# Kernel tuning notes

Measured on AMD Instinct MI355X. Metric: run time of the kernel, lower is better.

The kernel has to match this reference:

```python
import jax, jax.numpy as jnp
import numpy as np

N, E, D, H, C, L = 50000, 600000, 128, 128, 40, 2
NEG_SLOPE = 0.1


def setup_inputs() -> dict:
    key = jax.random.key(0)
    ks = jax.random.split(key, 12)

    def lin(k, din, dout):
        return (jax.random.normal(k, (din, dout), jnp.float32) / np.sqrt(din)).astype(jnp.float32)

    x = jax.random.normal(ks[0], (N, D), jnp.float32)
    edge_index = jax.random.randint(ks[1], (2, E), 0, N, dtype=jnp.int32)
    return {
        "x": x,
        "edge_index": edge_index,
        "enc_Wl": lin(ks[2], D, H),
        "enc_Wr": lin(ks[3], D, H),
        "enc_b": jnp.zeros((H,), jnp.float32),
        "lay_Wl": jnp.stack([lin(jax.random.fold_in(ks[4], i), H, H) for i in range(L)]),
        "lay_Wr": jnp.stack([lin(jax.random.fold_in(ks[5], i), H, H) for i in range(L)]),
        "lay_b": jnp.zeros((L, H), jnp.float32),
        "dec_Wl": lin(ks[6], H, C),
        "dec_Wr": lin(ks[7], H, C),
        "dec_b": jnp.zeros((C,), jnp.float32),
    }


def _sage(x, src, dst, inv_cnt, Wl, Wr, b):
    # mean-aggregate neighbor messages: gather x[src], scatter-sum to dst, divide by degree
    agg = jax.ops.segment_sum(x[src], dst, num_segments=N) * inv_cnt  # [N, d_in]
    return agg @ Wl + x @ Wr + b


def reference(x, edge_index, enc_Wl, enc_Wr, enc_b, lay_Wl, lay_Wr, lay_b, dec_Wl, dec_Wr, dec_b):
    src, dst = edge_index[0], edge_index[1]
    # in-degree per target node, clamped to 1 (PyG scatter-mean semantics: isolated nodes get 0)
    deg = jax.ops.segment_sum(jnp.ones((E,), jnp.float32), dst, num_segments=N)
    inv_cnt = (1.0 / jnp.maximum(deg, 1.0))[:, None]  # [N, 1]

    h = jax.nn.leaky_relu(_sage(x, src, dst, inv_cnt, enc_Wl, enc_Wr, enc_b), NEG_SLOPE)
    for i in range(L):
        h = jax.nn.leaky_relu(_sage(h, src, dst, inv_cnt, lay_Wl[i], lay_Wr[i], lay_b[i]), NEG_SLOPE)
    out = _sage(h, src, dst, inv_cnt, dec_Wl, dec_Wr, dec_b)
    return jax.nn.log_softmax(out, axis=1)
```

## Files before the change

### kernel.cpp

```cpp
#include <hip/hip_runtime.h>
#include <hip/hip_bf16.h>

#define NN 50000
#define EE 600000
#define HH 128
#define CC 40
#define NEG 0.1f
#define CAP 40

typedef __attribute__((ext_vector_type(8))) short bf16x8;
typedef __attribute__((ext_vector_type(4))) float f32x4;

__device__ __forceinline__ unsigned short f2bf(float f) {
    unsigned u = __float_as_uint(f);
    unsigned r = u + 0x7fffu + ((u >> 16) & 1u);
    return (unsigned short)(r >> 16);
}
__device__ __forceinline__ float bfhi(unsigned v) { return __uint_as_float(v & 0xFFFF0000u); }
__device__ __forceinline__ float bflo(unsigned v) { return __uint_as_float(v << 16); }

__global__ void k_build(const int* __restrict__ src, const int* __restrict__ dst,
                        int* __restrict__ counts, int* __restrict__ csr) {
    int e = blockIdx.x * blockDim.x + threadIdx.x;
    if (e < EE) {
        int d = dst[e];
        if ((unsigned)d < (unsigned)NN) {
            int sl = atomicAdd(&counts[d], 1);
            if (sl < CAP) csr[d * CAP + sl] = src[e];
        }
    }
}

struct PrepArgs {
    const float* wsrc[8];
    unsigned short* wdst[8];
    int* counts;
    const float* x;
    unsigned* xb;
};

template <int DOUT, int DOUTP>
__device__ __forceinline__ void swz_one(const float* __restrict__ W,
                                        unsigned short* __restrict__ dstf, int idx) {
    int k = idx / DOUTP, n = idx % DOUTP;
    unsigned short val = (n < DOUT) ? f2bf(W[k * DOUT + n]) : (unsigned short)0;
    int kt = k >> 5, kin = k & 31, nt = n >> 4, nin = n & 15;
    int lane = ((kin >> 3) << 4) | nin;
    int j = kin & 7;
    int NT = DOUTP >> 4;
    dstf[(((kt * NT + nt) * 64) + lane) * 8 + j] = val;
}

__global__ void k_prep(PrepArgs a) {
    int b = blockIdx.x;
    if (b < 384) {
        int tid = b * 256 + threadIdx.x;
        if (tid < NN) a.counts[tid] = 0;
        int which = b >> 6;
        int idx = (b & 63) * 256 + threadIdx.x;
        swz_one<HH, HH>(a.wsrc[which], a.wdst[which], idx);
    } else if (b < 432) {
        int bb = b - 384;
        int which = 6 + bb / 24;
        int idx = (bb % 24) * 256 + threadIdx.x;
        swz_one<CC, 48>(a.wsrc[which], a.wdst[which], idx);
    } else {
        int t = (b - 432) * 256 + threadIdx.x;
        if (t < NN * HH / 4) {
            float4 v = ((const float4*)a.x)[t];
            uint2 o;
            o.x = ((unsigned)f2bf(v.y) << 16) | f2bf(v.x);
            o.y = ((unsigned)f2bf(v.w) << 16) | f2bf(v.z);
            ((uint2*)a.xb)[t] = o;
        }
    }
}

template <int MODE>
__global__ __launch_bounds__(512) void k_layer(
    const unsigned short* __restrict__ hin,
    const int* __restrict__ counts, const int* __restrict__ csr,
    const unsigned short* __restrict__ B1f, const unsigned short* __restrict__ B2f,
    const float* __restrict__ bias, unsigned short* __restrict__ out,
    const unsigned short* __restrict__ Tf, unsigned short* __restrict__ tOut) {
    __shared__ unsigned lds[16][72];
    int wid = threadIdx.x >> 6;
    int lane = threadIdx.x & 63;
    int m0 = blockIdx.x * 16;
    int g = lane & 7;
    int s = lane >> 3;
    const uint4* hw4 = (const uint4*)hin;

    int beg[2], cnt[2];
    float sc[2];
    int maxd = 0;
#pragma unroll
    for (int n = 0; n < 2; ++n) {
        int node = m0 + wid * 2 + n;
        int c = counts[node];
        c = c < CAP ? c : CAP;
        beg[n] = node * CAP;
        cnt[n] = c;
        sc[n] = 1.0f / (float)(c > 0 ? c : 1);
        maxd = maxd > c ? maxd : c;
    }
    int rounds = (maxd + 7) >> 3;

    for (int ph = 0; ph < 2; ++ph) {
        float acc[2][8];
#pragma unroll
        for (int n = 0; n < 2; ++n)
#pragma unroll
            for (int d = 0; d < 8; ++d) acc[n][d] = 0.f;

        uint4 v[2]; int ok[2];
        auto issue = [&](int r, uint4* vv, int* okk) {
#pragma unroll
            for (int n = 0; n < 2; ++n) {
                int idx = r * 8 + s;
                int o = idx < cnt[n];
                int row = csr[beg[n] + (o ? idx : 0)];
                vv[n] = hw4[(size_t)row * 16 + ph * 8 + g];
                okk[n] = o;
            }
        };
        if (rounds > 0) {
            issue(0, v, ok);
            for (int r = 0; r < rounds; ++r) {
                uint4 vn[2]; int okn[2];
                bool more = (r + 1 < rounds);
                if (more) issue(r + 1, vn, okn);
#pragma unroll
                for (int n = 0; n < 2; ++n) {
                    if (ok[n]) {
                        acc[n][0] += bflo(v[n].x); acc[n][1] += bfhi(v[n].x);
                        acc[n][2] += bflo(v[n].y); acc[n][3] += bfhi(v[n].y);
                        acc[n][4] += bflo(v[n].z); acc[n][5] += bfhi(v[n].z);
                        acc[n][6] += bflo(v[n].w); acc[n][7] += bfhi(v[n].w);
                    }
                }
                if (more) {
#pragma unroll
                    for (int n = 0; n < 2; ++n) { v[n] = vn[n]; ok[n] = okn[n]; }
                }
            }
        }
#pragma unroll
        for (int n = 0; n < 2; ++n) {
#pragma unroll
            for (int d = 0; d < 8; ++d) {
                float t = acc[n][d];
                t += __shfl_xor(t, 8, 64);
                t += __shfl_xor(t, 16, 64);
                t += __shfl_xor(t, 32, 64);
                acc[n][d] = t;
            }
            if (s == 0) {
                uint4 w4;
                w4.x = ((unsigned)f2bf(acc[n][1] * sc[n]) << 16) | f2bf(acc[n][0] * sc[n]);
                w4.y = ((unsigned)f2bf(acc[n][3] * sc[n]) << 16) | f2bf(acc[n][2] * sc[n]);
                w4.z = ((unsigned)f2bf(acc[n][5] * sc[n]) << 16) | f2bf(acc[n][4] * sc[n]);
                w4.w = ((unsigned)f2bf(acc[n][7] * sc[n]) << 16) | f2bf(acc[n][6] * sc[n]);
                *(uint4*)&lds[wid * 2 + n][ph * 32 + g * 4] = w4;
            }
        }
    }
    __syncthreads();

    int nin = lane & 15;
    int kq = lane >> 4;
    const unsigned* arow = &lds[nin][0];

    f32x4 acc1 = (f32x4){0.f, 0.f, 0.f, 0.f};

#pragma unroll
    for (int kt = 0; kt < 4; ++kt) {
        bf16x8 a1 = *(const bf16x8*)(arow + kt * 16 + kq * 4);
        bf16x8 a2 = *(const bf16x8*)(hin + (size_t)(m0 + nin) * HH + kt * 32 + kq * 8);
        bf16x8 b1 = *(const bf16x8*)(B1f + (((kt * 8 + wid) * 64) + lane) * 8);
        acc1 = __builtin_amdgcn_mfma_f32_16x16x32_bf16(a1, b1, acc1, 0, 0, 0);
        bf16x8 b2 = *(const bf16x8*)(B2f + (((kt * 8 + wid) * 64) + lane) * 8);
        acc1 = __builtin_amdgcn_mfma_f32_16x16x32_bf16(a2, b2, acc1, 0, 0, 0);
    }

    int col = wid * 16 + nin;
    float bv = bias[col];
    unsigned short hv[4];
#pragma unroll
    for (int r = 0; r < 4; ++r) {
        int m = m0 + kq * 4 + r;
        float v = acc1[r] + bv;
        v = fmaxf(v, NEG * v);
        hv[r] = f2bf(v);
        out[(size_t)m * HH + col] = hv[r];
    }

    if (MODE == 1) {
        __syncthreads();
        unsigned short* lsh = (unsigned short*)&lds[0][0];
#pragma unroll
        for (int r = 0; r < 4; ++r) lsh[(kq * 4 + r) * 144 + col] = hv[r];
        __syncthreads();
        if (wid < 3) {
            f32x4 at = (f32x4){0.f, 0.f, 0.f, 0.f};
#pragma unroll
            for (int kt = 0; kt < 4; ++kt) {
                bf16x8 a = *(const bf16x8*)&lsh[nin * 144 + kt * 32 + kq * 8];
                bf16x8 b = *(const bf16x8*)(Tf + (((kt * 3 + wid) * 64) + lane) * 8);
                at = __builtin_amdgcn_mfma_f32_16x16x32_bf16(a, b, at, 0, 0, 0);
            }
#pragma unroll
            for (int r = 0; r < 4; ++r) {
                int m = m0 + kq * 4 + r;
                tOut[(size_t)m * 48 + wid * 16 + nin] = f2bf(at[r]);
            }
        }
    }
}

__global__ __launch_bounds__(512) void k_dec(
    const unsigned short* __restrict__ tbuf,
    const unsigned short* __restrict__ h1,
    const int* __restrict__ counts, const int* __restrict__ csr,
    const unsigned short* __restrict__ B2f, const float* __restrict__ bias,
    float* __restrict__ out) {
    __shared__ float aggT[16][52];
    int wid = threadIdx.x >> 6;
    int lane = threadIdx.x & 63;
    int m0 = blockIdx.x * 16;
    int g = lane & 7;
    int g6 = g < 6 ? g : g - 6;
    int s = lane >> 3;
    const uint4* t4 = (const uint4*)tbuf;

    int beg[2], cnt[2];
    float sc[2];
    int maxd = 0;
#pragma unroll
    for (int n = 0; n < 2; ++n) {
        int node = m0 + wid * 2 + n;
        int c = counts[node];
        c = c < CAP ? c : CAP;
        beg[n] = node * CAP;
        cnt[n] = c;
        sc[n] = 1.0f / (float)(c > 0 ? c : 1);
        maxd = maxd > c ? maxd : c;
    }
    int rounds = (maxd + 7) >> 3;

    float acc[2][8];
#pragma unroll
    for (int n = 0; n < 2; ++n)
#pragma unroll
        for (int d = 0; d < 8; ++d) acc[n][d] = 0.f;

    uint4 v[2]; int ok[2];
    auto issue = [&](int r, uint4* vv, int* okk) {
#pragma unroll
        for (int n = 0; n < 2; ++n) {
            int idx = r * 8 + s;
            int o = idx < cnt[n];
            int row = csr[beg[n] + (o ? idx : 0)];
            vv[n] = t4[(size_t)row * 6 + g6];
            okk[n] = o;
        }
    };
    if (rounds > 0) {
        issue(0, v, ok);
        for (int r = 0; r < rounds; ++r) {
            uint4 vn[2]; int okn[2];
            bool more = (r + 1 < rounds);
            if (more) issue(r + 1, vn, okn);
#pragma unroll
            for (int n = 0; n < 2; ++n) {
                if (ok[n]) {
                    acc[n][0] += bflo(v[n].x); acc[n][1] += bfhi(v[n].x);
                    acc[n][2] += bflo(v[n].y); acc[n][3] += bfhi(v[n].y);
                    acc[n][4] += bflo(v[n].z); acc[n][5] += bfhi(v[n].z);
                    acc[n][6] += bflo(v[n].w); acc[n][7] += bfhi(v[n].w);
                }
            }
            if (more) {
#pragma unroll
                for (int n = 0; n < 2; ++n) { v[n] = vn[n]; ok[n] = okn[n]; }
            }
        }
    }
#pragma unroll
    for (int n = 0; n < 2; ++n) {
#pragma unroll
        for (int d = 0; d < 8; ++d) {
            float t = acc[n][d];
            t += __shfl_xor(t, 8, 64);
            t += __shfl_xor(t, 16, 64);
            t += __shfl_xor(t, 32, 64);
            acc[n][d] = t;
        }
        if (s == 0 && g < 6) {
            float4 p0, p1;
            p0.x = acc[n][0] * sc[n]; p0.y = acc[n][1] * sc[n];
            p0.z = acc[n][2] * sc[n]; p0.w = acc[n][3] * sc[n];
            p1.x = acc[n][4] * sc[n]; p1.y = acc[n][5] * sc[n];
            p1.z = acc[n][6] * sc[n]; p1.w = acc[n][7] * sc[n];
            *(float4*)&aggT[wid * 2 + n][8 * g] = p0;
            *(float4*)&aggT[wid * 2 + n][8 * g + 4] = p1;
        }
    }
    __syncthreads();
    if (wid != 0) return;

    int nin = lane & 15, kq = lane >> 4;
    f32x4 acc2[3];
#pragma unroll
    for (int j = 0; j < 3; ++j) acc2[j] = (f32x4){0.f, 0.f, 0.f, 0.f};
#pragma unroll
    for (int kt = 0; kt < 4; ++kt) {
        bf16x8 a2 = *(const bf16x8*)(h1 + (size_t)(m0 + nin) * HH + kt * 32 + kq * 8);
#pragma unroll
        for (int j = 0; j < 3; ++j) {
            bf16x8 b2 = *(const bf16x8*)(B2f + (((kt * 3 + j) * 64) + lane) * 8);
            acc2[j] = __builtin_amdgcn_mfma_f32_16x16x32_bf16(a2, b2, acc2[j], 0, 0, 0);
        }
    }
    float bv[3];
#pragma unroll
    for (int t = 0; t < 3; ++t) {
        int col = t * 16 + nin;
        bv[t] = (col < CC) ? bias[col] : 0.f;
    }
#pragma unroll
    for (int r = 0; r < 4; ++r) {
        int m = m0 + kq * 4 + r;
        int ml = kq * 4 + r;
        float v[3];
        float mx = -1e30f;
#pragma unroll
        for (int t = 0; t < 3; ++t) {
            int col = t * 16 + nin;
            v[t] = acc2[t][r] + aggT[ml][col] + bv[t];
            if (col < CC) mx = fmaxf(mx, v[t]);
        }
        for (int off = 1; off < 16; off <<= 1) mx = fmaxf(mx, __shfl_xor(mx, off, 64));
        float sm = 0.f;
#pragma unroll
        for (int t = 0; t < 3; ++t) {
            int col = t * 16 + nin;
            if (col < CC) sm += expf(v[t] - mx);
        }
        for (int off = 1; off < 16; off <<= 1) sm += __shfl_xor(sm, off, 64);
        float lse = mx + logf(sm);
#pragma unroll
        for (int t = 0; t < 3; ++t) {
            int col = t * 16 + nin;
            if (col < CC) out[(size_t)m * CC + col] = v[t] - lse;
        }
    }
}

extern "C" void kernel_launch(void* const* d_in, const int* in_sizes, int n_in,
                              void* d_out, int out_size, void* d_ws, size_t ws_size,
                              hipStream_t stream) {
    const float* x      = (const float*)d_in[0];
    const int*   ei     = (const int*)d_in[1];
    const float* enc_Wl = (const float*)d_in[2];
    const float* enc_Wr = (const float*)d_in[3];
    const float* enc_b  = (const float*)d_in[4];
    const float* lay_Wl = (const float*)d_in[5];
    const float* lay_Wr = (const float*)d_in[6];
    const float* lay_b  = (const float*)d_in[7];
    const float* dec_Wl = (const float*)d_in[8];
    const float* dec_Wr = (const float*)d_in[9];
    const float* dec_b  = (const float*)d_in[10];
    float* out = (float*)d_out;

    const int* src = ei;
    const int* dst = ei + EE;

    char* p = (char*)d_ws;
    auto carve = [&](size_t bytes) {
        char* r = p;
        p += (bytes + 255) & ~(size_t)255;
        return r;
    };
    int*            counts = (int*)carve(NN * 4);
    int*            csr    = (int*)carve((size_t)NN * CAP * 4);
    unsigned short* h1     = (unsigned short*)carve((size_t)NN * HH * 2);
    unsigned short* h2     = (unsigned short*)carve((size_t)NN * HH * 2);
    unsigned short* tbuf   = (unsigned short*)carve((size_t)NN * 48 * 2 + 256);
    unsigned short* wf[8];
    for (int i = 0; i < 6; ++i) wf[i] = (unsigned short*)carve(HH * HH * 2);
    wf[6] = (unsigned short*)carve(HH * 48 * 2);
    wf[7] = (unsigned short*)carve(HH * 48 * 2);

    {
        PrepArgs a;
        a.wsrc[0] = enc_Wl; a.wsrc[1] = enc_Wr;
        a.wsrc[2] = lay_Wl; a.wsrc[3] = lay_Wr;
        a.wsrc[4] = lay_Wl + HH * HH; a.wsrc[5] = lay_Wr + HH * HH;
        a.wsrc[6] = dec_Wl; a.wsrc[7] = dec_Wr;
        for (int i = 0; i < 8; ++i) a.wdst[i] = wf[i];
        a.counts = counts;
        a.x = x;
        a.xb = (unsigned*)h2;
        k_prep<<<432 + (NN * HH / 4 + 255) / 256, 256, 0, stream>>>(a);
    }

    k_build<<<(EE + 255) / 256, 256, 0, stream>>>(src, dst, counts, csr);

    const int FB = NN / 16;
    k_layer<0><<<FB, 512, 0, stream>>>(h2, counts, csr, wf[0], wf[1], enc_b,      h1, nullptr, nullptr);
    k_layer<0><<<FB, 512, 0, stream>>>(h1, counts, csr, wf[2], wf[3], lay_b,      h2, nullptr, nullptr);
    k_layer<1><<<FB, 512, 0, stream>>>(h2, counts, csr, wf[4], wf[5], lay_b + HH, h1, wf[6], tbuf);

    k_dec<<<FB, 512, 0, stream>>>(tbuf, h1, counts, csr, wf[7], dec_b, out);
}
```

Baseline: 294.2 us.

## Assign one wavefront per node with fully unrolled prefetched neighbor gather

Blocks grow from 512 to 1024 threads, so each of the 16 wavefronts aggregates a single destination node instead of two. In k_layer each lane now reads a whole 256-byte row (16 lanes cover a row, 4 neighbors per round) in one pass rather than two half-row phases. All CSR indices are preloaded into registers and the gather is fully unrolled with three rotating buffers, replacing the dynamic loop bounded by the max degree of a node pair. This aims to raise memory-level parallelism and remove the phase loop and divergence between node pairs. The cost is that half the waves sit idle during the MFMA stage, plus higher register pressure under launch_bounds(1024, 8).

```diff
diff --git a/kernel.cpp b/kernel.cpp
--- a/kernel.cpp
+++ b/kernel.cpp
@@ -77,7 +77,7 @@
 }
 
 template <int MODE>
-__global__ __launch_bounds__(512) void k_layer(
+__global__ __launch_bounds__(1024, 8) void k_layer(
     const unsigned short* __restrict__ hin,
     const int* __restrict__ counts, const int* __restrict__ csr,
     const unsigned short* __restrict__ B1f, const unsigned short* __restrict__ B2f,
@@ -87,119 +87,111 @@
     int wid = threadIdx.x >> 6;
     int lane = threadIdx.x & 63;
     int m0 = blockIdx.x * 16;
-    int g = lane & 7;
-    int s = lane >> 3;
+    int gg = lane & 15;
+    int s = lane >> 4;
     const uint4* hw4 = (const uint4*)hin;
 
-    int beg[2], cnt[2];
-    float sc[2];
-    int maxd = 0;
-#pragma unroll
-    for (int n = 0; n < 2; ++n) {
-        int node = m0 + wid * 2 + n;
-        int c = counts[node];
-        c = c < CAP ? c : CAP;
-        beg[n] = node * CAP;
-        cnt[n] = c;
-        sc[n] = 1.0f / (float)(c > 0 ? c : 1);
-        maxd = maxd > c ? maxd : c;
-    }
-    int rounds = (maxd + 7) >> 3;
-
-    for (int ph = 0; ph < 2; ++ph) {
-        float acc[2][8];
-#pragma unroll
-        for (int n = 0; n < 2; ++n)
-#pragma unroll
-            for (int d = 0; d < 8; ++d) acc[n][d] = 0.f;
-
-        uint4 v[2]; int ok[2];
-        auto issue = [&](int r, uint4* vv, int* okk) {
-#pragma unroll
-            for (int n = 0; n < 2; ++n) {
-                int idx = r * 8 + s;
-                int o = idx < cnt[n];
-                int row = csr[beg[n] + (o ? idx : 0)];
-                vv[n] = hw4[(size_t)row * 16 + ph * 8 + g];
-                okk[n] = o;
-            }
-        };
-        if (rounds > 0) {
-            issue(0, v, ok);
-            for (int r = 0; r < rounds; ++r) {
-                uint4 vn[2]; int okn[2];
-                bool more = (r + 1 < rounds);
-                if (more) issue(r + 1, vn, okn);
-#pragma unroll
-                for (int n = 0; n < 2; ++n) {
-                    if (ok[n]) {
-                        acc[n][0] += bflo(v[n].x); acc[n][1] += bfhi(v[n].x);
-                        acc[n][2] += bflo(v[n].y); acc[n][3] += bfhi(v[n].y);
-                        acc[n][4] += bflo(v[n].z); acc[n][5] += bfhi(v[n].z);
-                        acc[n][6] += bflo(v[n].w); acc[n][7] += bfhi(v[n].w);
-                    }
-                }
-                if (more) {
-#pragma unroll
-                    for (int n = 0; n < 2; ++n) { v[n] = vn[n]; ok[n] = okn[n]; }
-                }
-            }
-        }
-#pragma unroll
-        for (int n = 0; n < 2; ++n) {
-#pragma unroll
-            for (int d = 0; d < 8; ++d) {
-                float t = acc[n][d];
-                t += __shfl_xor(t, 8, 64);
-                t += __shfl_xor(t, 16, 64);
-                t += __shfl_xor(t, 32, 64);
-                acc[n][d] = t;
-            }
-            if (s == 0) {
-                uint4 w4;
-                w4.x = ((unsigned)f2bf(acc[n][1] * sc[n]) << 16) | f2bf(acc[n][0] * sc[n]);
-                w4.y = ((unsigned)f2bf(acc[n][3] * sc[n]) << 16) | f2bf(acc[n][2] * sc[n]);
-                w4.z = ((unsigned)f2bf(acc[n][5] * sc[n]) << 16) | f2bf(acc[n][4] * sc[n]);
-                w4.w = ((unsigned)f2bf(acc[n][7] * sc[n]) << 16) | f2bf(acc[n][6] * sc[n]);
-                *(uint4*)&lds[wid * 2 + n][ph * 32 + g * 4] = w4;
-            }
-        }
+    int node = m0 + wid;
+    int cnt = counts[node];
+    cnt = cnt < CAP ? cnt : CAP;
+    int beg = node * CAP;
+    float sc = 1.0f / (float)(cnt > 0 ? cnt : 1);
+    int sr = (__builtin_amdgcn_readfirstlane(cnt) + 3) >> 2;
+
+    int row[10];
+#pragma unroll
+    for (int r = 0; r < 10; ++r) {
+        int v = csr[beg + r * 4 + s];
+        row[r] = ((unsigned)v < (unsigned)NN) ? v : 0;
+    }
+
+    float acc[8];
+#pragma unroll
+    for (int d = 0; d < 8; ++d) acc[d] = 0.f;
+
+    uint4 vA, vB, vC;
+
+#define ISS(R, V) \
+    if (sr > (R)) V = hw4[((unsigned)row[R] << 4) + gg]
+#define ACC8(R, V)                                            \
+    if (sr > (R)) {                                           \
+        if ((R) * 4 + s < cnt) {                              \
+            acc[0] += bflo(V.x); acc[1] += bfhi(V.x);         \
+            acc[2] += bflo(V.y); acc[3] += bfhi(V.y);         \
+            acc[4] += bflo(V.z); acc[5] += bfhi(V.z);         \
+            acc[6] += bflo(V.w); acc[7] += bfhi(V.w);         \
+        }                                                     \
+    }
+
+    ISS(0, vA); ISS(1, vB); ISS(2, vC);
+    ACC8(0, vA); ISS(3, vA);
+    ACC8(1, vB); ISS(4, vB);
+    ACC8(2, vC); ISS(5, vC);
+    ACC8(3, vA); ISS(6, vA);
+    ACC8(4, vB); ISS(7, vB);
+    ACC8(5, vC); ISS(8, vC);
+    ACC8(6, vA); ISS(9, vA);
+    ACC8(7, vB);
+    ACC8(8, vC);
+    ACC8(9, vA);
+#undef ISS
+#undef ACC8
+
+#pragma unroll
+    for (int d = 0; d < 8; ++d) {
+        float t = acc[d];
+        t += __shfl_xor(t, 16, 64);
+        t += __shfl_xor(t, 32, 64);
+        acc[d] = t * sc;
+    }
+    if (lane < 16) {
+        uint4 w4;
+        w4.x = ((unsigned)f2bf(acc[1]) << 16) | f2bf(acc[0]);
+        w4.y = ((unsigned)f2bf(acc[3]) << 16) | f2bf(acc[2]);
+        w4.z = ((unsigned)f2bf(acc[5]) << 16) | f2bf(acc[4]);
+        w4.w = ((unsigned)f2bf(acc[7]) << 16) | f2bf(acc[6]);
+        *(uint4*)&lds[wid][gg * 4] = w4;
     }
     __syncthreads();
 
     int nin = lane & 15;
     int kq = lane >> 4;
-    const unsigned* arow = &lds[nin][0];
-
-    f32x4 acc1 = (f32x4){0.f, 0.f, 0.f, 0.f};
-
-#pragma unroll
-    for (int kt = 0; kt < 4; ++kt) {
-        bf16x8 a1 = *(const bf16x8*)(arow + kt * 16 + kq * 4);
-        bf16x8 a2 = *(const bf16x8*)(hin + (size_t)(m0 + nin) * HH + kt * 32 + kq * 8);
-        bf16x8 b1 = *(const bf16x8*)(B1f + (((kt * 8 + wid) * 64) + lane) * 8);
-        acc1 = __builtin_amdgcn_mfma_f32_16x16x32_bf16(a1, b1, acc1, 0, 0, 0);
-        bf16x8 b2 = *(const bf16x8*)(B2f + (((kt * 8 + wid) * 64) + lane) * 8);
-        acc1 = __builtin_amdgcn_mfma_f32_16x16x32_bf16(a2, b2, acc1, 0, 0, 0);
-    }
-
-    int col = wid * 16 + nin;
-    float bv = bias[col];
     unsigned short hv[4];
-#pragma unroll
-    for (int r = 0; r < 4; ++r) {
-        int m = m0 + kq * 4 + r;
-        float v = acc1[r] + bv;
-        v = fmaxf(v, NEG * v);
-        hv[r] = f2bf(v);
-        out[(size_t)m * HH + col] = hv[r];
+
+    if (wid < 8) {
+        const unsigned* arow = &lds[nin][0];
+        f32x4 acc1 = (f32x4){0.f, 0.f, 0.f, 0.f};
+
+#pragma unroll
+        for (int kt = 0; kt < 4; ++kt) {
+            bf16x8 a1 = *(const bf16x8*)(arow + kt * 16 + kq * 4);
+            bf16x8 a2 = *(const bf16x8*)(hin + (size_t)(m0 + nin) * HH + kt * 32 + kq * 8);
+            bf16x8 b1 = *(const bf16x8*)(B1f + (((kt * 8 + wid) * 64) + lane) * 8);
+            acc1 = __builtin_amdgcn_mfma_f32_16x16x32_bf16(a1, b1, acc1, 0, 0, 0);
+            bf16x8 b2 = *(const bf16x8*)(B2f + (((kt * 8 + wid) * 64) + lane) * 8);
+            acc1 = __builtin_amdgcn_mfma_f32_16x16x32_bf16(a2, b2, acc1, 0, 0, 0);
+        }
+
+        int col = wid * 16 + nin;
+        float bv = bias[col];
+#pragma unroll
+        for (int r = 0; r < 4; ++r) {
+            int m = m0 + kq * 4 + r;
+            float v = acc1[r] + bv;
+            v = fmaxf(v, NEG * v);
+            hv[r] = f2bf(v);
+            out[(size_t)m * HH + col] = hv[r];
+        }
     }
 
     if (MODE == 1) {
         __syncthreads();
         unsigned short* lsh = (unsigned short*)&lds[0][0];
-#pragma unroll
-        for (int r = 0; r < 4; ++r) lsh[(kq * 4 + r) * 144 + col] = hv[r];
+        if (wid < 8) {
+            int col = wid * 16 + nin;
+#pragma unroll
+            for (int r = 0; r < 4; ++r) lsh[(kq * 4 + r) * 144 + col] = hv[r];
+        }
         __syncthreads();
         if (wid < 3) {
             f32x4 at = (f32x4){0.f, 0.f, 0.f, 0.f};
@@ -218,7 +210,7 @@
     }
 }
 
-__global__ __launch_bounds__(512) void k_dec(
+__global__ __launch_bounds__(1024, 8) void k_dec(
     const unsigned short* __restrict__ tbuf,
     const unsigned short* __restrict__ h1,
     const int* __restrict__ counts, const int* __restrict__ csr,
@@ -233,78 +225,61 @@
     int s = lane >> 3;
     const uint4* t4 = (const uint4*)tbuf;
 
-    int beg[2], cnt[2];
-    float sc[2];
-    int maxd = 0;
-#pragma unroll
-    for (int n = 0; n < 2; ++n) {
-        int node = m0 + wid * 2 + n;
-        int c = counts[node];
-        c = c < CAP ? c : CAP;
-        beg[n] = node * CAP;
-        cnt[n] = c;
-        sc[n] = 1.0f / (float)(c > 0 ? c : 1);
-        maxd = maxd > c ? maxd : c;
-    }
-    int rounds = (maxd + 7) >> 3;
-
-    float acc[2][8];
-#pragma unroll
-    for (int n = 0; n < 2; ++n)
-#pragma unroll
-        for (int d = 0; d < 8; ++d) acc[n][d] = 0.f;
-
-    uint4 v[2]; int ok[2];
-    auto issue = [&](int r, uint4* vv, int* okk) {
-#pragma unroll
-        for (int n = 0; n < 2; ++n) {
-            int idx = r * 8 + s;
-            int o = idx < cnt[n];
-            int row = csr[beg[n] + (o ? idx : 0)];
-            vv[n] = t4[(size_t)row * 6 + g6];
-            okk[n] = o;
-        }
-    };
-    if (rounds > 0) {
-        issue(0, v, ok);
-        for (int r = 0; r < rounds; ++r) {
-            uint4 vn[2]; int okn[2];
-            bool more = (r + 1 < rounds);
-            if (more) issue(r + 1, vn, okn);
-#pragma unroll
-            for (int n = 0; n < 2; ++n) {
-                if (ok[n]) {
-                    acc[n][0] += bflo(v[n].x); acc[n][1] += bfhi(v[n].x);
-                    acc[n][2] += bflo(v[n].y); acc[n][3] += bfhi(v[n].y);
-                    acc[n][4] += bflo(v[n].z); acc[n][5] += bfhi(v[n].z);
-                    acc[n][6] += bflo(v[n].w); acc[n][7] += bfhi(v[n].w);
-                }
-            }
-            if (more) {
-#pragma unroll
-                for (int n = 0; n < 2; ++n) { v[n] = vn[n]; ok[n] = okn[n]; }
-            }
-        }
-    }
-#pragma unroll
-    for (int n = 0; n < 2; ++n) {
-#pragma unroll
-        for (int d = 0; d < 8; ++d) {
-            float t = acc[n][d];
-            t += __shfl_xor(t, 8, 64);
-            t += __shfl_xor(t, 16, 64);
-            t += __shfl_xor(t, 32, 64);
-            acc[n][d] = t;
-        }
-        if (s == 0 && g < 6) {
-            float4 p0, p1;
-            p0.x = acc[n][0] * sc[n]; p0.y = acc[n][1] * sc[n];
-            p0.z = acc[n][2] * sc[n]; p0.w = acc[n][3] * sc[n];
-            p1.x = acc[n][4] * sc[n]; p1.y = acc[n][5] * sc[n];
-            p1.z = acc[n][6] * sc[n]; p1.w = acc[n][7] * sc[n];
-            *(float4*)&aggT[wid * 2 + n][8 * g] = p0;
-            *(float4*)&aggT[wid * 2 + n][8 * g + 4] = p1;
-        }
+    int node = m0 + wid;
+    int cnt = counts[node];
+    cnt = cnt < CAP ? cnt : CAP;
+    int beg = node * CAP;
+    float sc = 1.0f / (float)(cnt > 0 ? cnt : 1);
+    int sr = (__builtin_amdgcn_readfirstlane(cnt) + 7) >> 3;
+
+    int row[5];
+#pragma unroll
+    for (int r = 0; r < 5; ++r) {
+        int v = csr[beg + r * 8 + s];
+        row[r] = ((unsigned)v < (unsigned)NN) ? v : 0;
+    }
+
+    float acc[8];
+#pragma unroll
+    for (int d = 0; d < 8; ++d) acc[d] = 0.f;
+
+    uint4 vA, vB, vC;
+
+#define ISSD(R, V) \
+    if (sr > (R)) V = t4[(unsigned)row[R] * 6 + g6]
+#define ACCD(R, V)                                            \
+    if (sr > (R)) {                                           \
+        if ((R) * 8 + s < cnt) {                              \
+            acc[0] += bflo(V.x); acc[1] += bfhi(V.x);         \
+            acc[2] += bflo(V.y); acc[3] += bfhi(V.y);         \
+            acc[4] += bflo(V.z); acc[5] += bfhi(V.z);         \
+            acc[6] += bflo(V.w); acc[7] += bfhi(V.w);         \
+        }                                                     \
+    }
+
+    ISSD(0, vA); ISSD(1, vB); ISSD(2, vC);
+    ACCD(0, vA); ISSD(3, vA);
+    ACCD(1, vB); ISSD(4, vB);
+    ACCD(2, vC);
+    ACCD(3, vA);
+    ACCD(4, vB);
+#undef ISSD
+#undef ACCD
+
+#pragma unroll
+    for (int d = 0; d < 8; ++d) {
+        float t = acc[d];
+        t += __shfl_xor(t, 8, 64);
+        t += __shfl_xor(t, 16, 64);
+        t += __shfl_xor(t, 32, 64);
+        acc[d] = t * sc;
+    }
+    if (s == 0 && g < 6) {
+        float4 p0, p1;
+        p0.x = acc[0]; p0.y = acc[1]; p0.z = acc[2]; p0.w = acc[3];
+        p1.x = acc[4]; p1.y = acc[5]; p1.z = acc[6]; p1.w = acc[7];
+        *(float4*)&aggT[wid][8 * g] = p0;
+        *(float4*)&aggT[wid][8 * g + 4] = p1;
     }
     __syncthreads();
     if (wid != 0) return;
@@ -408,9 +383,9 @@
     k_build<<<(EE + 255) / 256, 256, 0, stream>>>(src, dst, counts, csr);
 
     const int FB = NN / 16;
-    k_layer<0><<<FB, 512, 0, stream>>>(h2, counts, csr, wf[0], wf[1], enc_b,      h1, nullptr, nullptr);
-    k_layer<0><<<FB, 512, 0, stream>>>(h1, counts, csr, wf[2], wf[3], lay_b,      h2, nullptr, nullptr);
-    k_layer<1><<<FB, 512, 0, stream>>>(h2, counts, csr, wf[4], wf[5], lay_b + HH, h1, wf[6], tbuf);
-
-    k_dec<<<FB, 512, 0, stream>>>(tbuf, h1, counts, csr, wf[7], dec_b, out);
-}
+    k_layer<0><<<FB, 1024, 0, stream>>>(h2, counts, csr, wf[0], wf[1], enc_b,      h1, nullptr, nullptr);
+    k_layer<0><<<FB, 1024, 0, stream>>>(h1, counts, csr, wf[2], wf[3], lay_b,      h2, nullptr, nullptr);
+    k_layer<1><<<FB, 1024, 0, stream>>>(h2, counts, csr, wf[4], wf[5], lay_b + HH, h1, wf[6], tbuf);
+
+    k_dec<<<FB, 1024, 0, stream>>>(tbuf, h1, counts, csr, wf[7], dec_b, out);
+}
```

New measurement: 295.7 us. About the same (+0.5%).
